# Kernel tuning notes

Hardware: AMD Instinct MI355X
Metric: run time of the kernel (lower is better)

The kernel has to match this reference:

```python
import jax, jax.numpy as jnp
import numpy as np

B, K, D = 1024, 262144, 64

def setup_inputs() -> dict:
    key = jax.random.key(0)
    k1, k2 = jax.random.split(key)
    query_vec = jax.random.normal(k1, (B, D), dtype=jnp.float32)
    memory = jax.random.normal(k2, (K, D), dtype=jnp.float32)
    return {"query_vec": query_vec, "memory": memory, "topk": 5}

def reference(query_vec, memory, topk):
    # sim: [B, K] similarity against the full memory bank
    sim = jnp.einsum('bd,kd->bk', query_vec, memory)
    # indices of top-k most similar bank rows: [B, topk]
    _, topk_idx = jax.lax.top_k(sim, topk)
    # gather rows: [B, topk, D]
    return memory[topk_idx]
```

## Files before the change

### kernel.cpp

```cpp
#include <hip/hip_runtime.h>
#include <stdint.h>

typedef unsigned long long u64;
typedef __attribute__((ext_vector_type(8))) short short8;
typedef __attribute__((ext_vector_type(4))) float f32x4;

#define KROWS  262144
#define DDIM   64
#define NQ     1024
#define NC     256
#define CHUNK  (KROWS / NC)
#define SUB    128
#define NSUB   (CHUNK / SUB)
#define KC_PER 4
#define BIAS   128.0f
#define SIMMASK 0xFFFFFC00u

#define WSK_BYTES   ((size_t)NQ * NC * KC_PER * 4)
#define MB_BYTES    ((size_t)KROWS * DDIM * 2)

__device__ __forceinline__ uint32_t ord32(float f) {
    uint32_t u = __float_as_uint(f);
    return (u & 0x80000000u) ? ~u : (u | 0x80000000u);
}
__device__ __forceinline__ uint32_t maxu(uint32_t a, uint32_t b) { return a > b ? a : b; }
__device__ __forceinline__ uint32_t minu(uint32_t a, uint32_t b) { return a < b ? a : b; }
__device__ __forceinline__ void fold2(uint32_t& t0, uint32_t& t1, uint32_t k) {
    t1 = maxu(t1, minu(t0, k));
    t0 = maxu(t0, k);
}
__device__ __forceinline__ void fold4(uint32_t (&t)[4], uint32_t k) {
    uint32_t n1 = maxu(t[1], minu(t[0], k));
    uint32_t n2 = maxu(t[2], minu(t[1], k));
    uint32_t n3 = maxu(t[3], minu(t[2], k));
    t[0] = maxu(t[0], k);
    t[1] = n1; t[2] = n2; t[3] = n3;
}
__device__ __forceinline__ uint32_t cvtpk(float a, float b) {
    uint32_t r;
    asm("v_cvt_pk_bf16_f32 %0, %1, %2" : "=v"(r) : "v"(a), "v"(b));
    return r;
}
__device__ __forceinline__ void gl_lds16(const uint16_t* g, uint16_t* l) {
    __builtin_amdgcn_global_load_lds(
        (const __attribute__((address_space(1))) void*)g,
        (__attribute__((address_space(3))) void*)l, 16, 0, 0);
}

__global__ __launch_bounds__(256) void pc(const float* __restrict__ Mf,
                                          uint16_t* __restrict__ Mb) {
    const int g = blockIdx.x * 256 + threadIdx.x;
    const int row = (g >> 3) & 127;
    const int cl  = g & 7;
    const int cg  = cl ^ (row & 7);
    const size_t R = ((size_t)(g >> 10)) * 128 + (size_t)row;
    const float* src = Mf + R * DDIM + cg * 8;
    const float4 f0 = ((const float4*)src)[0];
    const float4 f1 = ((const float4*)src)[1];
    uint4 wv;
    wv.x = cvtpk(f0.x, f0.y); wv.y = cvtpk(f0.z, f0.w);
    wv.z = cvtpk(f1.x, f1.y); wv.w = cvtpk(f1.z, f1.w);
    *(uint4*)(Mb + (size_t)g * 8) = wv;
}

template<bool PRE>
__global__ __launch_bounds__(512)
__attribute__((amdgpu_waves_per_eu(4, 8)))
void p1(const float* __restrict__ Qg,
        const float* __restrict__ Mf,
        const uint16_t* __restrict__ Mb,
        uint32_t* __restrict__ wsK) {
    __shared__ __align__(16) uint16_t stage[2 * 8192];
    const int t = threadIdx.x;
    const int lane = t & 63;
    const int w = t >> 6;
    const int quad = lane >> 4;
    const int m = lane & 15;
    const int qcol = blockIdx.x;
    const int chunk = blockIdx.y;
    const int qBase = qcol * 256 + w * 32;
    const int rowChunk = chunk * CHUNK;

    short8 afr[2][2];
    #pragma unroll
    for (int qt = 0; qt < 2; ++qt)
        #pragma unroll
        for (int kh = 0; kh < 2; ++kh) {
            const float* qp = Qg + (size_t)(qBase + qt * 16 + m) * DDIM + quad * 8 + kh * 32;
            const float4 f0 = ((const float4*)qp)[0];
            const float4 f1 = ((const float4*)qp)[1];
            union { short8 s; uint32_t u[4]; } cv;
            cv.u[0] = cvtpk(f0.x, f0.y);
            cv.u[1] = cvtpk(f0.z, f0.w);
            cv.u[2] = cvtpk(f1.x, f1.y);
            cv.u[3] = cvtpk(f1.z, f1.w);
            afr[qt][kh] = cv.s;
        }
    const f32x4 bias = {BIAS, BIAS, BIAS, BIAS};

    uint32_t tA[8], tB[8];
    #pragma unroll
    for (int li = 0; li < 8; ++li) { tA[li] = 0u; tB[li] = 0u; }

    const int sr0 = t >> 3;
    const int sc0 = (t & 7) ^ (sr0 & 7);
    const uint16_t* mbBase = PRE ? (Mb + ((size_t)chunk * 8) * 8192) : nullptr;

    auto stage_sub = [&](int sb, int buf) {
        if (PRE) {
            const uint16_t* s0 = mbBase + (size_t)sb * 8192;
            uint16_t* d0 = stage + buf * 8192;
            gl_lds16(s0 + (size_t)t * 8,         d0 + (size_t)t * 8);
            gl_lds16(s0 + (size_t)(t + 512) * 8, d0 + (size_t)(t + 512) * 8);
        } else {
            const float* base = Mf + (size_t)(rowChunk + sb * SUB + sr0) * DDIM + sc0 * 8;
            const float4 a0 = ((const float4*)base)[0];
            const float4 a1 = ((const float4*)base)[1];
            const float4 b0 = ((const float4*)(base + 64 * DDIM))[0];
            const float4 b1 = ((const float4*)(base + 64 * DDIM))[1];
            uint16_t* bp = stage + buf * 8192;
            uint4 w0, w1;
            w0.x = cvtpk(a0.x, a0.y); w0.y = cvtpk(a0.z, a0.w);
            w0.z = cvtpk(a1.x, a1.y); w0.w = cvtpk(a1.z, a1.w);
            w1.x = cvtpk(b0.x, b0.y); w1.y = cvtpk(b0.z, b0.w);
            w1.z = cvtpk(b1.x, b1.y); w1.w = cvtpk(b1.z, b1.w);
            *(uint4*)(bp + (size_t)t * 8) = w0;
            *(uint4*)(bp + (size_t)(t + 512) * 8) = w1;
        }
    };

    stage_sub(0, 0);
    #pragma unroll 2
    for (int sb = 0; sb < NSUB; ++sb) {
        __syncthreads();
        if (sb + 1 < NSUB) stage_sub(sb + 1, (sb + 1) & 1);
        const uint16_t* bufp = stage + (sb & 1) * 8192;
        const uint32_t pb = (uint32_t)m + (uint32_t)sb * 128u;
        #pragma unroll
        for (int rt = 0; rt < 8; ++rt) {
            const int r = rt * 16 + m;
            const short8 v0 = *(const short8*)(bufp + r * 64 + ((quad       ^ (m & 7)) * 8));
            const short8 v1 = *(const short8*)(bufp + r * 64 + (((quad + 4) ^ (m & 7)) * 8));
            f32x4 c0, c1;
            c0 = __builtin_amdgcn_mfma_f32_16x16x32_bf16(afr[0][0], v0, bias, 0, 0, 0);
            c0 = __builtin_amdgcn_mfma_f32_16x16x32_bf16(afr[0][1], v1, c0,   0, 0, 0);
            c1 = __builtin_amdgcn_mfma_f32_16x16x32_bf16(afr[1][0], v0, bias, 0, 0, 0);
            c1 = __builtin_amdgcn_mfma_f32_16x16x32_bf16(afr[1][1], v1, c1,   0, 0, 0);
            const uint32_t posm = pb + (uint32_t)(rt * 16);
            #pragma unroll
            for (int reg = 0; reg < 4; ++reg) {
                fold2(tA[reg],     tB[reg],     (__float_as_uint(c0[reg]) & SIMMASK) | posm);
                fold2(tA[4 + reg], tB[4 + reg], (__float_as_uint(c1[reg]) & SIMMASK) | posm);
            }
        }
    }

    #pragma unroll
    for (int g = 0; g < 2; ++g) {
        uint32_t fl[4][4];
        #pragma unroll
        for (int r4 = 0; r4 < 4; ++r4) {
            fl[r4][0] = tA[g * 4 + r4]; fl[r4][1] = tB[g * 4 + r4];
            fl[r4][2] = 0u;             fl[r4][3] = 0u;
        }
        #pragma unroll
        for (int d = 1; d <= 8; d <<= 1) {
            const int nv = (d == 1) ? 2 : 4;
            #pragma unroll
            for (int r4 = 0; r4 < 4; ++r4) {
                uint32_t rm[4];
                #pragma unroll
                for (int s = 0; s < 4; ++s)
                    if (s < nv) rm[s] = __shfl_xor(fl[r4][s], d, 64);
                #pragma unroll
                for (int s = 0; s < 4; ++s)
                    if (s < nv) fold4(fl[r4], rm[s]);
            }
        }
        if (m == 0) {
            #pragma unroll
            for (int r4 = 0; r4 < 4; ++r4) {
                const int q = qBase + g * 16 + quad * 4 + r4;
                uint4 v4; v4.x = fl[r4][0]; v4.y = fl[r4][1];
                v4.z = fl[r4][2]; v4.w = fl[r4][3];
                *(uint4*)(wsK + ((size_t)q * NC + (size_t)chunk) * KC_PER) = v4;
            }
        }
    }
}

__global__ __launch_bounds__(256) void p2(const float* __restrict__ Qg,
                                          const float* __restrict__ Mf,
                                          const uint32_t* __restrict__ wsK,
                                          float* __restrict__ out) {
    __shared__ uint32_t candRow[64];
    __shared__ u64 candScore[64];
    const int Q = blockIdx.x;
    const int t = threadIdx.x;
    const int lane = t & 63;
    const int w = t >> 6;

    const int c = w * 64 + lane;
    const uint4 k4 = *(const uint4*)(wsK + ((size_t)Q * NC + (size_t)c) * KC_PER);
    uint32_t s[16];
    s[0] = (k4.x & SIMMASK) | ((uint32_t)lane << 2) | 0u;
    s[1] = (k4.y & SIMMASK) | ((uint32_t)lane << 2) | 1u;
    s[2] = (k4.z & SIMMASK) | ((uint32_t)lane << 2) | 2u;
    s[3] = (k4.w & SIMMASK) | ((uint32_t)lane << 2) | 3u;
    #pragma unroll
    for (int i = 4; i < 16; ++i) s[i] = 0u;

    #pragma unroll
    for (int d = 1; d <= 32; d <<= 1) {
        uint32_t r[16];
        #pragma unroll
        for (int i = 0; i < 16; ++i) r[i] = __shfl_xor(s[i], d, 64);
        uint32_t mm[16];
        #pragma unroll
        for (int i = 0; i < 16; ++i) mm[i] = maxu(s[i], r[15 - i]);
        #pragma unroll
        for (int dd = 8; dd >= 1; dd >>= 1) {
            #pragma unroll
            for (int i = 0; i < 16; ++i) {
                if ((i & dd) == 0) {
                    const uint32_t hi = maxu(mm[i], mm[i + dd]);
                    const uint32_t lo = minu(mm[i], mm[i + dd]);
                    mm[i] = hi; mm[i + dd] = lo;
                }
            }
        }
        #pragma unroll
        for (int i = 0; i < 16; ++i) s[i] = mm[i];
    }

    uint32_t ck = s[0];
    #pragma unroll
    for (int j = 1; j < 16; ++j) ck = (lane == j) ? s[j] : ck;
    if (lane < 16) {
        const int srcLane = (int)((ck >> 2) & 63u);
        const int jj = (int)(ck & 3u);
        const int c2 = w * 64 + srcLane;
        const uint32_t raw = wsK[((size_t)Q * NC + (size_t)c2) * KC_PER + jj];
        candRow[w * 16 + lane] = (uint32_t)c2 * (uint32_t)CHUNK + (raw & 1023u);
    }
    __syncthreads();

    const float qv = Qg[(size_t)Q * DDIM + lane];
    #pragma unroll
    for (int j = 0; j < 16; ++j) {
        const uint32_t grow = candRow[w * 16 + j];
        const float v = Mf[(size_t)grow * DDIM + lane];
        float p = qv * v;
        #pragma unroll
        for (int off = 32; off >= 1; off >>= 1) p += __shfl_xor(p, off, 64);
        if (lane == 0)
            candScore[w * 16 + j] = ((u64)ord32(p) << 32) | (u64)(~grow);
    }
    __syncthreads();

    if (w == 0) {
        u64 key = candScore[lane];
        #pragma unroll
        for (int it = 0; it < 5; ++it) {
            u64 best = key;
            #pragma unroll
            for (int off = 32; off >= 1; off >>= 1) {
                const u64 o = __shfl_xor(best, off, 64);
                best = o > best ? o : best;
            }
            const uint32_t wrow = ~(uint32_t)best;
            out[((size_t)Q * 5 + it) * DDIM + lane] = Mf[(size_t)wrow * DDIM + lane];
            key = (key == best) ? 0ull : key;
        }
    }
}

extern "C" void kernel_launch(void* const* d_in, const int* in_sizes, int n_in,
                              void* d_out, int out_size, void* d_ws, size_t ws_size,
                              hipStream_t stream) {
    const float* Qg = (const float*)d_in[0];
    const float* Mf = (const float*)d_in[1];
    float* out = (float*)d_out;
    uint32_t* wsK = (uint32_t*)d_ws;

    if (ws_size >= WSK_BYTES + MB_BYTES) {
        uint16_t* Mb = (uint16_t*)((char*)d_ws + WSK_BYTES);
        pc<<<(KROWS * DDIM / 8) / 256, 256, 0, stream>>>(Mf, Mb);
        p1<true><<<dim3(4, NC), 512, 0, stream>>>(Qg, Mf, Mb, wsK);
    } else {
        p1<false><<<dim3(4, NC), 512, 0, stream>>>(Qg, Mf, nullptr, wsK);
    }
    p2<<<NQ, 256, 0, stream>>>(Qg, Mf, wsK, out);
}
```

Measured before the change: 178.1 us.

## Read bf16 memory bank directly from global into MFMA operands, bypassing LDS staging

The precomputed bf16 bank path now uses a new kernel that loads MFMA B-fragments straight from global memory in a plain row-major layout. This drops the double-buffered LDS staging, the barriers and the XOR swizzle. The grid is also reordered so the chunk index is the fast dimension, which lets the four query-column blocks sharing a chunk run close together and reuse it through cache. The trade-off is uncoalesced 16-byte per-lane global loads with no explicit prefetch, so memory latency may be exposed more directly.

```diff
diff --git a/kernel.cpp b/kernel.cpp
--- a/kernel.cpp
+++ b/kernel.cpp
@@ -41,20 +41,11 @@
     asm("v_cvt_pk_bf16_f32 %0, %1, %2" : "=v"(r) : "v"(a), "v"(b));
     return r;
 }
-__device__ __forceinline__ void gl_lds16(const uint16_t* g, uint16_t* l) {
-    __builtin_amdgcn_global_load_lds(
-        (const __attribute__((address_space(1))) void*)g,
-        (__attribute__((address_space(3))) void*)l, 16, 0, 0);
-}
 
 __global__ __launch_bounds__(256) void pc(const float* __restrict__ Mf,
                                           uint16_t* __restrict__ Mb) {
     const int g = blockIdx.x * 256 + threadIdx.x;
-    const int row = (g >> 3) & 127;
-    const int cl  = g & 7;
-    const int cg  = cl ^ (row & 7);
-    const size_t R = ((size_t)(g >> 10)) * 128 + (size_t)row;
-    const float* src = Mf + R * DDIM + cg * 8;
+    const float* src = Mf + (size_t)g * 8;
     const float4 f0 = ((const float4*)src)[0];
     const float4 f1 = ((const float4*)src)[1];
     uint4 wv;
@@ -63,13 +54,99 @@
     *(uint4*)(Mb + (size_t)g * 8) = wv;
 }
 
-template<bool PRE>
+__global__ __launch_bounds__(512)
+void p1pre(const float* __restrict__ Qg,
+           const uint16_t* __restrict__ Mb,
+           uint32_t* __restrict__ wsK) {
+    const int t = threadIdx.x;
+    const int lane = t & 63;
+    const int w = t >> 6;
+    const int quad = lane >> 4;
+    const int m = lane & 15;
+    const int chunk = blockIdx.x;
+    const int qcol = blockIdx.y;
+    const int qBase = qcol * 256 + w * 32;
+
+    short8 afr[2][2];
+    #pragma unroll
+    for (int qt = 0; qt < 2; ++qt)
+        #pragma unroll
+        for (int kh = 0; kh < 2; ++kh) {
+            const float* qp = Qg + (size_t)(qBase + qt * 16 + m) * DDIM + quad * 8 + kh * 32;
+            const float4 f0 = ((const float4*)qp)[0];
+            const float4 f1 = ((const float4*)qp)[1];
+            union { short8 s; uint32_t u[4]; } cv;
+            cv.u[0] = cvtpk(f0.x, f0.y);
+            cv.u[1] = cvtpk(f0.z, f0.w);
+            cv.u[2] = cvtpk(f1.x, f1.y);
+            cv.u[3] = cvtpk(f1.z, f1.w);
+            afr[qt][kh] = cv.s;
+        }
+    const f32x4 bias = {BIAS, BIAS, BIAS, BIAS};
+
+    uint32_t tA[8], tB[8];
+    #pragma unroll
+    for (int li = 0; li < 8; ++li) { tA[li] = 0u; tB[li] = 0u; }
+
+    const uint16_t* mrow = Mb + ((size_t)chunk * CHUNK + (size_t)m) * DDIM + quad * 8;
+
+    #pragma unroll 4
+    for (int j = 0; j < 64; ++j) {
+        const uint16_t* p = mrow + (size_t)j * 16 * DDIM;
+        const short8 v0 = *(const short8*)(p);
+        const short8 v1 = *(const short8*)(p + 32);
+        f32x4 c0, c1;
+        c0 = __builtin_amdgcn_mfma_f32_16x16x32_bf16(afr[0][0], v0, bias, 0, 0, 0);
+        c0 = __builtin_amdgcn_mfma_f32_16x16x32_bf16(afr[0][1], v1, c0,   0, 0, 0);
+        c1 = __builtin_amdgcn_mfma_f32_16x16x32_bf16(afr[1][0], v0, bias, 0, 0, 0);
+        c1 = __builtin_amdgcn_mfma_f32_16x16x32_bf16(afr[1][1], v1, c1,   0, 0, 0);
+        const uint32_t posm = (uint32_t)m + (uint32_t)(j * 16);
+        #pragma unroll
+        for (int reg = 0; reg < 4; ++reg) {
+            fold2(tA[reg],     tB[reg],     (__float_as_uint(c0[reg]) & SIMMASK) | posm);
+            fold2(tA[4 + reg], tB[4 + reg], (__float_as_uint(c1[reg]) & SIMMASK) | posm);
+        }
+    }
+
+    #pragma unroll
+    for (int g = 0; g < 2; ++g) {
+        uint32_t fl[4][4];
+        #pragma unroll
+        for (int r4 = 0; r4 < 4; ++r4) {
+            fl[r4][0] = tA[g * 4 + r4]; fl[r4][1] = tB[g * 4 + r4];
+            fl[r4][2] = 0u;             fl[r4][3] = 0u;
+        }
+        #pragma unroll
+        for (int d = 1; d <= 8; d <<= 1) {
+            const int nv = (d == 1) ? 2 : 4;
+            #pragma unroll
+            for (int r4 = 0; r4 < 4; ++r4) {
+                uint32_t rm[4];
+                #pragma unroll
+                for (int s = 0; s < 4; ++s)
+                    if (s < nv) rm[s] = __shfl_xor(fl[r4][s], d, 64);
+                #pragma unroll
+                for (int s = 0; s < 4; ++s)
+                    if (s < nv) fold4(fl[r4], rm[s]);
+            }
+        }
+        if (m == 0) {
+            #pragma unroll
+            for (int r4 = 0; r4 < 4; ++r4) {
+                const int q = qBase + g * 16 + quad * 4 + r4;
+                uint4 v4; v4.x = fl[r4][0]; v4.y = fl[r4][1];
+                v4.z = fl[r4][2]; v4.w = fl[r4][3];
+                *(uint4*)(wsK + ((size_t)q * NC + (size_t)chunk) * KC_PER) = v4;
+            }
+        }
+    }
+}
+
 __global__ __launch_bounds__(512)
 __attribute__((amdgpu_waves_per_eu(4, 8)))
-void p1(const float* __restrict__ Qg,
-        const float* __restrict__ Mf,
-        const uint16_t* __restrict__ Mb,
-        uint32_t* __restrict__ wsK) {
+void p1lds(const float* __restrict__ Qg,
+           const float* __restrict__ Mf,
+           uint32_t* __restrict__ wsK) {
     __shared__ __align__(16) uint16_t stage[2 * 8192];
     const int t = threadIdx.x;
     const int lane = t & 63;
@@ -104,29 +181,20 @@
 
     const int sr0 = t >> 3;
     const int sc0 = (t & 7) ^ (sr0 & 7);
-    const uint16_t* mbBase = PRE ? (Mb + ((size_t)chunk * 8) * 8192) : nullptr;
-
     auto stage_sub = [&](int sb, int buf) {
-        if (PRE) {
-            const uint16_t* s0 = mbBase + (size_t)sb * 8192;
-            uint16_t* d0 = stage + buf * 8192;
-            gl_lds16(s0 + (size_t)t * 8,         d0 + (size_t)t * 8);
-            gl_lds16(s0 + (size_t)(t + 512) * 8, d0 + (size_t)(t + 512) * 8);
-        } else {
-            const float* base = Mf + (size_t)(rowChunk + sb * SUB + sr0) * DDIM + sc0 * 8;
-            const float4 a0 = ((const float4*)base)[0];
-            const float4 a1 = ((const float4*)base)[1];
-            const float4 b0 = ((const float4*)(base + 64 * DDIM))[0];
-            const float4 b1 = ((const float4*)(base + 64 * DDIM))[1];
-            uint16_t* bp = stage + buf * 8192;
-            uint4 w0, w1;
-            w0.x = cvtpk(a0.x, a0.y); w0.y = cvtpk(a0.z, a0.w);
-            w0.z = cvtpk(a1.x, a1.y); w0.w = cvtpk(a1.z, a1.w);
-            w1.x = cvtpk(b0.x, b0.y); w1.y = cvtpk(b0.z, b0.w);
-            w1.z = cvtpk(b1.x, b1.y); w1.w = cvtpk(b1.z, b1.w);
-            *(uint4*)(bp + (size_t)t * 8) = w0;
-            *(uint4*)(bp + (size_t)(t + 512) * 8) = w1;
-        }
+        const float* base = Mf + (size_t)(rowChunk + sb * SUB + sr0) * DDIM + sc0 * 8;
+        const float4 a0 = ((const float4*)base)[0];
+        const float4 a1 = ((const float4*)base)[1];
+        const float4 b0 = ((const float4*)(base + 64 * DDIM))[0];
+        const float4 b1 = ((const float4*)(base + 64 * DDIM))[1];
+        uint16_t* bp = stage + buf * 8192;
+        uint4 w0, w1;
+        w0.x = cvtpk(a0.x, a0.y); w0.y = cvtpk(a0.z, a0.w);
+        w0.z = cvtpk(a1.x, a1.y); w0.w = cvtpk(a1.z, a1.w);
+        w1.x = cvtpk(b0.x, b0.y); w1.y = cvtpk(b0.z, b0.w);
+        w1.z = cvtpk(b1.x, b1.y); w1.w = cvtpk(b1.z, b1.w);
+        *(uint4*)(bp + (size_t)t * 8) = w0;
+        *(uint4*)(bp + (size_t)(t + 512) * 8) = w1;
     };
 
     stage_sub(0, 0);
@@ -286,9 +354,9 @@
     if (ws_size >= WSK_BYTES + MB_BYTES) {
         uint16_t* Mb = (uint16_t*)((char*)d_ws + WSK_BYTES);
         pc<<<(KROWS * DDIM / 8) / 256, 256, 0, stream>>>(Mf, Mb);
-        p1<true><<<dim3(4, NC), 512, 0, stream>>>(Qg, Mf, Mb, wsK);
+        p1pre<<<dim3(NC, 4), 512, 0, stream>>>(Qg, Mb, wsK);
     } else {
-        p1<false><<<dim3(4, NC), 512, 0, stream>>>(Qg, Mf, nullptr, wsK);
+        p1lds<<<dim3(4, NC), 512, 0, stream>>>(Qg, Mf, wsK);
     }
     p2<<<NQ, 256, 0, stream>>>(Qg, Mf, wsK, out);
 }
```

Result: slower. 241.7 us (+35.7%).
